# Kernel optimization log

Measured on AMD Instinct MI355X. Metric: run time of the kernel, lower is better.

Reference implementation:

```python
import jax, jax.numpy as jnp
import numpy as np

B, S, D, H = 2, 2048, 1024, 16
HD = D // H

def setup_inputs() -> dict:
    key = jax.random.key(0)
    ks = jax.random.split(key, 9)
    s = 1.0 / np.sqrt(D)
    return {
        "x": jax.random.normal(ks[0], (B, S, D), jnp.float32),
        "Wq": jax.random.normal(ks[1], (D, D), jnp.float32) * s,
        "bq": jnp.zeros((D,), jnp.float32),
        "Wk": jax.random.normal(ks[2], (D, D), jnp.float32) * s,
        "bk": jnp.zeros((D,), jnp.float32),
        "Wv": jax.random.normal(ks[3], (D, D), jnp.float32) * s,
        "bv": jnp.zeros((D,), jnp.float32),
        "Wo": jax.random.normal(ks[4], (D, D), jnp.float32) * s,
        "bo": jnp.zeros((D,), jnp.float32),
    }

def reference(x, Wq, bq, Wk, bk, Wv, bv, Wo, bo):
    b, s, d = x.shape
    def split_heads(t):
        return t.reshape(b, s, H, HD).transpose(0, 2, 1, 3)  # [B,H,S,HD]
    q = split_heads(x @ Wq + bq)
    k = split_heads(x @ Wk + bk)
    v = split_heads(x @ Wv + bv)
    scores = jnp.einsum('bhqd,bhkd->bhqk', q, k) / jnp.sqrt(jnp.float32(HD))
    causal = jnp.tril(jnp.ones((s, s), bool))  # True = keep
    scores = jnp.where(causal, scores, -jnp.inf)
    attn = jax.nn.softmax(scores, axis=-1)
    out = jnp.einsum('bhqk,bhkd->bhqd', attn, v)  # [B,H,S,HD]
    out = out.transpose(0, 2, 1, 3).reshape(b, s, d)
    return out @ Wo + bo
```

## Files before the change

kernel.cpp:

```cpp
#include <hip/hip_runtime.h>

typedef unsigned short u16;
typedef unsigned int u32;
typedef __attribute__((ext_vector_type(8))) short bf16x8;
typedef __attribute__((ext_vector_type(4))) float f32x4;

#define BB 2
#define SS 2048
#define DD 1024
#define HH 16
#define HD 64
#define MM (BB * SS)

__device__ inline float u2f(u32 u) { return __uint_as_float(u); }
__device__ inline u16 f2bf(float f) {
  u32 u = __float_as_uint(f);
  return (u16)((u + 0x7fffu + ((u >> 16) & 1u)) >> 16);
}

__global__ __launch_bounds__(256) void prep(const float* __restrict__ x, u16* __restrict__ xb,
                                            const float* __restrict__ W0, const float* __restrict__ W1,
                                            const float* __restrict__ W2, const float* __restrict__ W3,
                                            u16* __restrict__ Wt) {
  int z = blockIdx.z;
  int t = threadIdx.x;
  if (z >= 4) {
    int gid = (z - 4) * 256 + blockIdx.y * 16 + blockIdx.x;
    int i = (gid * 256 + t) * 8;
    float4 a = *(const float4*)(x + i);
    float4 b = *(const float4*)(x + i + 4);
    uint4 o;
    o.x = (u32)f2bf(a.x) | ((u32)f2bf(a.y) << 16);
    o.y = (u32)f2bf(a.z) | ((u32)f2bf(a.w) << 16);
    o.z = (u32)f2bf(b.x) | ((u32)f2bf(b.y) << 16);
    o.w = (u32)f2bf(b.z) | ((u32)f2bf(b.w) << 16);
    *(uint4*)(xb + i) = o;
    return;
  }
  const float* W = (z == 0) ? W0 : (z == 1) ? W1 : (z == 2) ? W2 : W3;
  u16* out = Wt + (size_t)z * (DD * DD);
  __shared__ __align__(16) u16 T[64][72];
  int n0 = blockIdx.x * 64, k0 = blockIdx.y * 64;
#pragma unroll
  for (int p = 0; p < 4; ++p) {
    int kr = (t >> 4) + p * 16;
    int c4 = (t & 15) * 4;
    float4 v = *(const float4*)&W[(size_t)(k0 + kr) * DD + n0 + c4];
    T[c4 + 0][kr] = f2bf(v.x);
    T[c4 + 1][kr] = f2bf(v.y);
    T[c4 + 2][kr] = f2bf(v.z);
    T[c4 + 3][kr] = f2bf(v.w);
  }
  __syncthreads();
#pragma unroll
  for (int p = 0; p < 2; ++p) {
    int n = (t >> 3) + p * 32;
    int c8 = (t & 7) * 8;
    uint4 v = *(const uint4*)&T[n][c8];
    *(uint4*)&out[(size_t)(n0 + n) * DD + k0 + c8] = v;
  }
}

__global__ __launch_bounds__(256) void gemm_qkv(const u16* __restrict__ xb, const u16* __restrict__ Wt,
                                                const float* __restrict__ bq, const float* __restrict__ bk,
                                                const float* __restrict__ bv,
                                                u16* __restrict__ Qb, u16* __restrict__ Kb, u16* __restrict__ Vtb) {
  __shared__ __align__(16) u16 As[2][128 * 32];
  __shared__ __align__(16) u16 Bs[2][128 * 32];
  const int tid = threadIdx.x, lane = tid & 63, wv = tid >> 6;
  const int wm = (wv >> 1) * 64, wn = (wv & 1) * 64;
  const int l16 = lane & 15, quad = lane >> 4;
  int z = blockIdx.z;
  const u16* Bt = Wt + (size_t)z * (DD * DD);
  const float* bias = (z == 0) ? bq : (z == 1) ? bk : bv;
  int m0 = blockIdx.y * 128, n0 = blockIdx.x * 128;

  const int r0 = tid >> 2, k8 = (tid & 3) << 3;
  const u16* Ap0 = &xb[(size_t)(m0 + r0) * DD + k8];
  const u16* Ap1 = Ap0 + (size_t)64 * DD;
  const u16* Bp0 = &Bt[(size_t)(n0 + r0) * DD + k8];
  const u16* Bp1 = Bp0 + (size_t)64 * DD;

  uint4 a0 = *(const uint4*)Ap0, a1 = *(const uint4*)Ap1;
  uint4 b0 = *(const uint4*)Bp0, b1 = *(const uint4*)Bp1;
  *(uint4*)&As[0][r0 * 32 + k8] = a0;
  *(uint4*)&As[0][(r0 + 64) * 32 + k8] = a1;
  *(uint4*)&Bs[0][r0 * 32 + k8] = b0;
  *(uint4*)&Bs[0][(r0 + 64) * 32 + k8] = b1;
  a0 = *(const uint4*)(Ap0 + 32);
  a1 = *(const uint4*)(Ap1 + 32);
  b0 = *(const uint4*)(Bp0 + 32);
  b1 = *(const uint4*)(Bp1 + 32);
  __syncthreads();

  f32x4 acc[4][4];
  f32x4 zero = {0.f, 0.f, 0.f, 0.f};
#pragma unroll
  for (int i = 0; i < 4; ++i)
#pragma unroll
    for (int j = 0; j < 4; ++j) acc[i][j] = zero;

  for (int kk = 0; kk < 32; ++kk) {
    const int cur = (kk & 1) * 4096;
    bf16x8 af[4], bg[4];
#pragma unroll
    for (int i = 0; i < 4; ++i) {
      af[i] = *(const bf16x8*)&As[0][cur + (wm + i * 16 + l16) * 32 + quad * 8];
      bg[i] = *(const bf16x8*)&Bs[0][cur + (wn + i * 16 + l16) * 32 + quad * 8];
    }
#pragma unroll
    for (int i = 0; i < 4; ++i)
#pragma unroll
      for (int j = 0; j < 4; ++j)
        acc[i][j] = __builtin_amdgcn_mfma_f32_16x16x32_bf16(af[i], bg[j], acc[i][j], 0, 0, 0);
    if (kk + 1 < 32) {
      const int nxt = 4096 - cur;
      *(uint4*)&As[0][nxt + r0 * 32 + k8] = a0;
      *(uint4*)&As[0][nxt + (r0 + 64) * 32 + k8] = a1;
      *(uint4*)&Bs[0][nxt + r0 * 32 + k8] = b0;
      *(uint4*)&Bs[0][nxt + (r0 + 64) * 32 + k8] = b1;
      if (kk + 2 < 32) {
        int ko = (kk + 2) * 32;
        a0 = *(const uint4*)(Ap0 + ko);
        a1 = *(const uint4*)(Ap1 + ko);
        b0 = *(const uint4*)(Bp0 + ko);
        b1 = *(const uint4*)(Bp1 + ko);
      }
    }
    __syncthreads();
  }

  const float qsc = (z == 0) ? 0.180336880f : 1.0f;
  if (z == 2) {
#pragma unroll
    for (int i = 0; i < 4; ++i) {
#pragma unroll
      for (int j = 0; j < 4; ++j) {
        int col = n0 + wn + j * 16 + l16;
        float bcol = bias[col];
        int hh = col >> 6, dd = col & 63;
        int row0 = m0 + wm + i * 16 + quad * 4;
        int bb = row0 >> 11, s0 = row0 & (SS - 1);
        u32 w0 = (u32)f2bf(acc[i][j][0] + bcol) | ((u32)f2bf(acc[i][j][1] + bcol) << 16);
        u32 w1 = (u32)f2bf(acc[i][j][2] + bcol) | ((u32)f2bf(acc[i][j][3] + bcol) << 16);
        uint2 pk; pk.x = w0; pk.y = w1;
        *(uint2*)&Vtb[(((size_t)((bb * HH + hh) * HD + dd)) << 11) + s0] = pk;
      }
    }
  } else {
    u16* out = (z == 0) ? Qb : Kb;
#pragma unroll
    for (int i = 0; i < 4; ++i) {
#pragma unroll
      for (int j = 0; j < 4; ++j) {
        int col = n0 + wn + j * 16 + l16;
        float bcol = bias[col];
        int hh = col >> 6, dd = col & 63;
#pragma unroll
        for (int r = 0; r < 4; ++r) {
          int row = m0 + wm + i * 16 + quad * 4 + r;
          int bb = row >> 11, s = row & (SS - 1);
          out[((size_t)((bb * HH + hh) * SS + s) << 6) | dd] = f2bf((acc[i][j][r] + bcol) * qsc);
        }
      }
    }
  }
}

__global__ __launch_bounds__(256) void gemm_out(const u16* __restrict__ Ub, const u16* __restrict__ Wot,
                                                const float* __restrict__ bo, float* __restrict__ out) {
  __shared__ __align__(16) u16 As[2][128 * 32];
  __shared__ __align__(16) u16 Bs[2][64 * 32];
  const int tid = threadIdx.x, lane = tid & 63, wv = tid >> 6;
  const int wm = (wv >> 1) * 64, wn = (wv & 1) * 32;
  const int l16 = lane & 15, quad = lane >> 4;
  const int r0 = tid >> 2, k8 = (tid & 3) << 3;
  int m0 = blockIdx.y * 128, n0 = blockIdx.x * 64;

  const u16* Ap0 = &Ub[(size_t)(m0 + r0) * DD + k8];
  const u16* Ap1 = Ap0 + (size_t)64 * DD;
  const u16* Bp0 = &Wot[(size_t)(n0 + r0) * DD + k8];

  uint4 a0 = *(const uint4*)Ap0, a1 = *(const uint4*)Ap1, b0 = *(const uint4*)Bp0;
  *(uint4*)&As[0][r0 * 32 + k8] = a0;
  *(uint4*)&As[0][(r0 + 64) * 32 + k8] = a1;
  *(uint4*)&Bs[0][r0 * 32 + k8] = b0;
  a0 = *(const uint4*)(Ap0 + 32);
  a1 = *(const uint4*)(Ap1 + 32);
  b0 = *(const uint4*)(Bp0 + 32);
  __syncthreads();

  f32x4 acc[4][2];
  f32x4 zero = {0.f, 0.f, 0.f, 0.f};
#pragma unroll
  for (int i = 0; i < 4; ++i) { acc[i][0] = zero; acc[i][1] = zero; }

  for (int kk = 0; kk < 32; ++kk) {
    const int curA = (kk & 1) * 4096, curB = (kk & 1) * 2048;
    bf16x8 af[4], bg[2];
#pragma unroll
    for (int i = 0; i < 4; ++i) af[i] = *(const bf16x8*)&As[0][curA + (wm + i * 16 + l16) * 32 + quad * 8];
#pragma unroll
    for (int j = 0; j < 2; ++j) bg[j] = *(const bf16x8*)&Bs[0][curB + (wn + j * 16 + l16) * 32 + quad * 8];
#pragma unroll
    for (int i = 0; i < 4; ++i)
#pragma unroll
      for (int j = 0; j < 2; ++j)
        acc[i][j] = __builtin_amdgcn_mfma_f32_16x16x32_bf16(af[i], bg[j], acc[i][j], 0, 0, 0);
    if (kk + 1 < 32) {
      const int nxtA = 4096 - curA, nxtB = 2048 - curB;
      *(uint4*)&As[0][nxtA + r0 * 32 + k8] = a0;
      *(uint4*)&As[0][nxtA + (r0 + 64) * 32 + k8] = a1;
      *(uint4*)&Bs[0][nxtB + r0 * 32 + k8] = b0;
      if (kk + 2 < 32) {
        int ko = (kk + 2) * 32;
        a0 = *(const uint4*)(Ap0 + ko);
        a1 = *(const uint4*)(Ap1 + ko);
        b0 = *(const uint4*)(Bp0 + ko);
      }
    }
    __syncthreads();
  }

#pragma unroll
  for (int i = 0; i < 4; ++i) {
#pragma unroll
    for (int j = 0; j < 2; ++j) {
      int col = n0 + wn + j * 16 + l16;
      float bcol = bo[col];
#pragma unroll
      for (int r = 0; r < 4; ++r) {
        int row = m0 + wm + i * 16 + quad * 4 + r;
        out[(size_t)row * DD + col] = acc[i][j][r] + bcol;
      }
    }
  }
}

__global__ __launch_bounds__(256, 2) void attention_mfma(const u16* __restrict__ Q, const u16* __restrict__ K,
                                                         const u16* __restrict__ Vt, u16* __restrict__ Uo) {
  const int tid = threadIdx.x, lane = tid & 63, wv = tid >> 6;
  const int l16 = lane & 15, quad = lane >> 4;
  const int h = blockIdx.y, b = blockIdx.z;
  const int qA = blockIdx.x;
  const int qB = 31 - qA;
  const int q0A = qA * 64, q0B = qB * 64;
  const u16* Qh = Q + (size_t)(b * HH + h) * SS * HD;
  const u16* Kh = K + (size_t)(b * HH + h) * SS * HD;
  const u16* Vh = Vt + (size_t)(b * HH + h) * HD * SS;

  __shared__ __align__(16) u16 K_lds[2][64][72];
  __shared__ __align__(16) u16 V_lds[2][64][72];
  __shared__ __align__(16) u16 p_lds[2][64][72];

  bf16x8 qfA0, qfA1, qfB0, qfB1;
  {
    const u16* qa = &Qh[(size_t)(q0A + wv * 16 + l16) * HD + quad * 8];
    qfA0 = *(const bf16x8*)qa;
    qfA1 = *(const bf16x8*)(qa + 32);
    const u16* qb = &Qh[(size_t)(q0B + wv * 16 + l16) * HD + quad * 8];
    qfB0 = *(const bf16x8*)qb;
    qfB1 = *(const bf16x8*)(qb + 32);
  }

  f32x4 zero = {0.f, 0.f, 0.f, 0.f};
  f32x4 oA[4], oB[4];
#pragma unroll
  for (int j = 0; j < 4; ++j) { oA[j] = zero; oB[j] = zero; }
  float lA[4] = {0.f, 0.f, 0.f, 0.f}, lB[4] = {0.f, 0.f, 0.f, 0.f};

  const int sr = tid >> 2, cc = (tid & 3) << 3;
  const u16* Kg = &Kh[(size_t)sr * HD + cc];
  const u16* Vg = &Vh[(size_t)sr * SS + cc];
  const int ktiles = qB + 1;

  uint4 ka = *(const uint4*)Kg, kb = *(const uint4*)(Kg + 32);
  uint4 va = *(const uint4*)Vg, vb = *(const uint4*)(Vg + 32);
  *(uint4*)&K_lds[0][sr][cc] = ka;
  *(uint4*)&K_lds[0][sr][cc + 32] = kb;
  *(uint4*)&V_lds[0][sr][cc] = va;
  *(uint4*)&V_lds[0][sr][cc + 32] = vb;
  {
    const u16* Kn = Kg + (size_t)64 * HD;
    const u16* Vn = Vg + 64;
    ka = *(const uint4*)Kn; kb = *(const uint4*)(Kn + 32);
    va = *(const uint4*)Vn; vb = *(const uint4*)(Vn + 32);
  }
  __syncthreads();

  for (int t = 0; t < ktiles; ++t) {
    const int cur = t & 1;
    const bool doA = (t <= qA);

    f32x4 sA[4], sB[4];
#pragma unroll
    for (int n = 0; n < 4; ++n) {
      bf16x8 kf0 = *(const bf16x8*)&K_lds[cur][n * 16 + l16][quad * 8];
      bf16x8 kf1 = *(const bf16x8*)&K_lds[cur][n * 16 + l16][32 + quad * 8];
      f32x4 aB = zero;
      aB = __builtin_amdgcn_mfma_f32_16x16x32_bf16(qfB0, kf0, aB, 0, 0, 0);
      aB = __builtin_amdgcn_mfma_f32_16x16x32_bf16(qfB1, kf1, aB, 0, 0, 0);
      sB[n] = aB;
      if (doA) {
        f32x4 aA = zero;
        aA = __builtin_amdgcn_mfma_f32_16x16x32_bf16(qfA0, kf0, aA, 0, 0, 0);
        aA = __builtin_amdgcn_mfma_f32_16x16x32_bf16(qfA1, kf1, aA, 0, 0, 0);
        sA[n] = aA;
      }
    }

    {
      const int rel = q0B + wv * 16 + quad * 4 - t * 64;
#pragma unroll
      for (int rr = 0; rr < 4; ++rr) {
        float p0 = __builtin_amdgcn_exp2f(sB[0][rr]);
        float p1 = __builtin_amdgcn_exp2f(sB[1][rr]);
        float p2 = __builtin_amdgcn_exp2f(sB[2][rr]);
        float p3 = __builtin_amdgcn_exp2f(sB[3][rr]);
        if (t == qB) {
          int row = rel + rr;
          p0 = (l16 <= row) ? p0 : 0.f;
          p1 = (16 + l16 <= row) ? p1 : 0.f;
          p2 = (32 + l16 <= row) ? p2 : 0.f;
          p3 = (48 + l16 <= row) ? p3 : 0.f;
        }
        lB[rr] += (p0 + p1) + (p2 + p3);
        u16* pr = p_lds[1][wv * 16 + quad * 4 + rr];
        pr[l16]      = (u16)(__float_as_uint(p0) >> 16);
        pr[16 + l16] = (u16)(__float_as_uint(p1) >> 16);
        pr[32 + l16] = (u16)(__float_as_uint(p2) >> 16);
        pr[48 + l16] = (u16)(__float_as_uint(p3) >> 16);
      }
    }
    if (doA) {
      const int rel = q0A + wv * 16 + quad * 4 - t * 64;
#pragma unroll
      for (int rr = 0; rr < 4; ++rr) {
        float p0 = __builtin_amdgcn_exp2f(sA[0][rr]);
        float p1 = __builtin_amdgcn_exp2f(sA[1][rr]);
        float p2 = __builtin_amdgcn_exp2f(sA[2][rr]);
        float p3 = __builtin_amdgcn_exp2f(sA[3][rr]);
        if (t == qA) {
          int row = rel + rr;
          p0 = (l16 <= row) ? p0 : 0.f;
          p1 = (16 + l16 <= row) ? p1 : 0.f;
          p2 = (32 + l16 <= row) ? p2 : 0.f;
          p3 = (48 + l16 <= row) ? p3 : 0.f;
        }
        lA[rr] += (p0 + p1) + (p2 + p3);
        u16* pr = p_lds[0][wv * 16 + quad * 4 + rr];
        pr[l16]      = (u16)(__float_as_uint(p0) >> 16);
        pr[16 + l16] = (u16)(__float_as_uint(p1) >> 16);
        pr[32 + l16] = (u16)(__float_as_uint(p2) >> 16);
        pr[48 + l16] = (u16)(__float_as_uint(p3) >> 16);
      }
    }

    if (doA) {
      bf16x8 pB0 = *(const bf16x8*)&p_lds[1][wv * 16 + l16][quad * 8];
      bf16x8 pB1 = *(const bf16x8*)&p_lds[1][wv * 16 + l16][32 + quad * 8];
      bf16x8 pA0 = *(const bf16x8*)&p_lds[0][wv * 16 + l16][quad * 8];
      bf16x8 pA1 = *(const bf16x8*)&p_lds[0][wv * 16 + l16][32 + quad * 8];
#pragma unroll
      for (int j = 0; j < 4; ++j) {
        bf16x8 vf0 = *(const bf16x8*)&V_lds[cur][j * 16 + l16][quad * 8];
        bf16x8 vf1 = *(const bf16x8*)&V_lds[cur][j * 16 + l16][32 + quad * 8];
        oB[j] = __builtin_amdgcn_mfma_f32_16x16x32_bf16(pB0, vf0, oB[j], 0, 0, 0);
        oB[j] = __builtin_amdgcn_mfma_f32_16x16x32_bf16(pB1, vf1, oB[j], 0, 0, 0);
        oA[j] = __builtin_amdgcn_mfma_f32_16x16x32_bf16(pA0, vf0, oA[j], 0, 0, 0);
        oA[j] = __builtin_amdgcn_mfma_f32_16x16x32_bf16(pA1, vf1, oA[j], 0, 0, 0);
      }
    } else {
      bf16x8 pB0 = *(const bf16x8*)&p_lds[1][wv * 16 + l16][quad * 8];
      bf16x8 pB1 = *(const bf16x8*)&p_lds[1][wv * 16 + l16][32 + quad * 8];
#pragma unroll
      for (int j = 0; j < 4; ++j) {
        bf16x8 vf0 = *(const bf16x8*)&V_lds[cur][j * 16 + l16][quad * 8];
        bf16x8 vf1 = *(const bf16x8*)&V_lds[cur][j * 16 + l16][32 + quad * 8];
        oB[j] = __builtin_amdgcn_mfma_f32_16x16x32_bf16(pB0, vf0, oB[j], 0, 0, 0);
        oB[j] = __builtin_amdgcn_mfma_f32_16x16x32_bf16(pB1, vf1, oB[j], 0, 0, 0);
      }
    }

    if (t + 1 < ktiles) {
      const int nxt = cur ^ 1;
      *(uint4*)&K_lds[nxt][sr][cc] = ka;
      *(uint4*)&K_lds[nxt][sr][cc + 32] = kb;
      *(uint4*)&V_lds[nxt][sr][cc] = va;
      *(uint4*)&V_lds[nxt][sr][cc + 32] = vb;
      if (t + 2 < ktiles) {
        const u16* Kn = Kg + (size_t)(t + 2) * 64 * HD;
        const u16* Vn = Vg + (t + 2) * 64;
        ka = *(const uint4*)Kn; kb = *(const uint4*)(Kn + 32);
        va = *(const uint4*)Vn; vb = *(const uint4*)(Vn + 32);
      }
    }
    __syncthreads();
  }

#pragma unroll
  for (int rr = 0; rr < 4; ++rr) {
    float a = lA[rr], c = lB[rr];
#pragma unroll
    for (int off = 1; off < 16; off <<= 1) {
      a += __shfl_xor(a, off);
      c += __shfl_xor(c, off);
    }
    lA[rr] = 1.0f / a;
    lB[rr] = 1.0f / c;
  }

#pragma unroll
  for (int j = 0; j < 4; ++j) {
#pragma unroll
    for (int r = 0; r < 4; ++r) {
      int rowA = q0A + wv * 16 + quad * 4 + r;
      int rowB = q0B + wv * 16 + quad * 4 + r;
      Uo[(size_t)(b * SS + rowA) * DD + (h << 6) + j * 16 + l16] = f2bf(oA[j][r] * lA[r]);
      Uo[(size_t)(b * SS + rowB) * DD + (h << 6) + j * 16 + l16] = f2bf(oB[j][r] * lB[r]);
    }
  }
}

extern "C" void kernel_launch(void* const* d_in, const int* in_sizes, int n_in,
                              void* d_out, int out_size, void* d_ws, size_t ws_size,
                              hipStream_t stream) {
  const float* x  = (const float*)d_in[0];
  const float* Wq = (const float*)d_in[1];
  const float* bq = (const float*)d_in[2];
  const float* Wk = (const float*)d_in[3];
  const float* bk = (const float*)d_in[4];
  const float* Wv = (const float*)d_in[5];
  const float* bv = (const float*)d_in[6];
  const float* Wo = (const float*)d_in[7];
  const float* bo = (const float*)d_in[8];
  float* out = (float*)d_out;

  char* ws = (char*)d_ws;
  u16* xb  = (u16*)(ws);
  u16* Wt  = (u16*)(ws + ((size_t)8 << 20));
  u16* Qb  = (u16*)(ws + ((size_t)16 << 20));
  u16* Kb  = (u16*)(ws + ((size_t)24 << 20));
  u16* Vtb = (u16*)(ws + ((size_t)32 << 20));
  u16* Ub  = (u16*)(ws + ((size_t)40 << 20));

  prep<<<dim3(16, 16, 12), dim3(256), 0, stream>>>(x, xb, Wq, Wk, Wv, Wo, Wt);
  gemm_qkv<<<dim3(8, 32, 3), dim3(256), 0, stream>>>(xb, Wt, bq, bk, bv, Qb, Kb, Vtb);
  attention_mfma<<<dim3(16, 16, 2), dim3(256), 0, stream>>>(Qb, Kb, Vtb, Ub);
  gemm_out<<<dim3(16, 32), dim3(256), 0, stream>>>(Ub, Wt + (size_t)3 * DD * DD, bo, out);
}
```

Baseline: 189.8 us.

## Remap blocks for XCD-aware L2 locality, swizzle attention K/V LDS, raise occupancy

Flattens the grids of both GEMMs and the attention kernel and decodes block ids so that tiles sharing the same A or B panels, or the same batch-head, land on the same XCD. The aim is better L2 reuse across the MI355X's chiplets. The attention K/V shared tiles drop the padded 72-wide rows for an XOR-swizzled 64-wide layout, which cuts LDS footprint and avoids bank conflicts. Launch bounds are raised to 3 blocks per CU, which may force register spills.

```diff
diff --git a/kernel.cpp b/kernel.cpp
--- a/kernel.cpp
+++ b/kernel.cpp
@@ -17,6 +17,8 @@
   u32 u = __float_as_uint(f);
   return (u16)((u + 0x7fffu + ((u >> 16) & 1u)) >> 16);
 }
+
+__device__ inline int sw(int r, int ci) { return r * 64 + (((ci ^ (r & 7)) & 7) << 3); }
 
 __global__ __launch_bounds__(256) void prep(const float* __restrict__ x, u16* __restrict__ xb,
                                             const float* __restrict__ W0, const float* __restrict__ W1,
@@ -61,19 +63,25 @@
   }
 }
 
-__global__ __launch_bounds__(256) void gemm_qkv(const u16* __restrict__ xb, const u16* __restrict__ Wt,
-                                                const float* __restrict__ bq, const float* __restrict__ bk,
-                                                const float* __restrict__ bv,
-                                                u16* __restrict__ Qb, u16* __restrict__ Kb, u16* __restrict__ Vtb) {
+__global__ __launch_bounds__(256, 3) void gemm_qkv(const u16* __restrict__ xb, const u16* __restrict__ Wt,
+                                                   const float* __restrict__ bq, const float* __restrict__ bk,
+                                                   const float* __restrict__ bv,
+                                                   u16* __restrict__ Qb, u16* __restrict__ Kb, u16* __restrict__ Vtb) {
   __shared__ __align__(16) u16 As[2][128 * 32];
   __shared__ __align__(16) u16 Bs[2][128 * 32];
   const int tid = threadIdx.x, lane = tid & 63, wv = tid >> 6;
   const int wm = (wv >> 1) * 64, wn = (wv & 1) * 64;
   const int l16 = lane & 15, quad = lane >> 4;
-  int z = blockIdx.z;
+
+  const int id = blockIdx.x;
+  const int xcd = id & 7, inner = id >> 3;
+  const int mg = xcd >> 1, ng = xcd & 1;
+  const int im = inner & 7, rest = inner >> 3;
+  const int in_ = rest & 3, z = rest >> 2;
+  const int m0 = (mg * 8 + im) * 128, n0 = (ng * 4 + in_) * 128;
+
   const u16* Bt = Wt + (size_t)z * (DD * DD);
   const float* bias = (z == 0) ? bq : (z == 1) ? bk : bv;
-  int m0 = blockIdx.y * 128, n0 = blockIdx.x * 128;
 
   const int r0 = tid >> 2, k8 = (tid & 3) << 3;
   const u16* Ap0 = &xb[(size_t)(m0 + r0) * DD + k8];
@@ -167,15 +175,20 @@
   }
 }
 
-__global__ __launch_bounds__(256) void gemm_out(const u16* __restrict__ Ub, const u16* __restrict__ Wot,
-                                                const float* __restrict__ bo, float* __restrict__ out) {
+__global__ __launch_bounds__(256, 3) void gemm_out(const u16* __restrict__ Ub, const u16* __restrict__ Wot,
+                                                   const float* __restrict__ bo, float* __restrict__ out) {
   __shared__ __align__(16) u16 As[2][128 * 32];
   __shared__ __align__(16) u16 Bs[2][64 * 32];
   const int tid = threadIdx.x, lane = tid & 63, wv = tid >> 6;
   const int wm = (wv >> 1) * 64, wn = (wv & 1) * 32;
   const int l16 = lane & 15, quad = lane >> 4;
   const int r0 = tid >> 2, k8 = (tid & 3) << 3;
-  int m0 = blockIdx.y * 128, n0 = blockIdx.x * 64;
+
+  const int id = blockIdx.x;
+  const int xcd = id & 7, inner = id >> 3;
+  const int mg = xcd >> 1, ng = xcd & 1;
+  const int im = inner & 7, in_ = inner >> 3;
+  const int m0 = (mg * 8 + im) * 128, n0 = (ng * 8 + in_) * 64;
 
   const u16* Ap0 = &Ub[(size_t)(m0 + r0) * DD + k8];
   const u16* Ap1 = Ap0 + (size_t)64 * DD;
@@ -237,20 +250,21 @@
   }
 }
 
-__global__ __launch_bounds__(256, 2) void attention_mfma(const u16* __restrict__ Q, const u16* __restrict__ K,
+__global__ __launch_bounds__(256, 3) void attention_mfma(const u16* __restrict__ Q, const u16* __restrict__ K,
                                                          const u16* __restrict__ Vt, u16* __restrict__ Uo) {
   const int tid = threadIdx.x, lane = tid & 63, wv = tid >> 6;
   const int l16 = lane & 15, quad = lane >> 4;
-  const int h = blockIdx.y, b = blockIdx.z;
-  const int qA = blockIdx.x;
+  const int bh = blockIdx.x & 31;
+  const int b = bh >> 4, h = bh & 15;
+  const int qA = blockIdx.x >> 5;
   const int qB = 31 - qA;
   const int q0A = qA * 64, q0B = qB * 64;
   const u16* Qh = Q + (size_t)(b * HH + h) * SS * HD;
   const u16* Kh = K + (size_t)(b * HH + h) * SS * HD;
   const u16* Vh = Vt + (size_t)(b * HH + h) * HD * SS;
 
-  __shared__ __align__(16) u16 K_lds[2][64][72];
-  __shared__ __align__(16) u16 V_lds[2][64][72];
+  __shared__ __align__(16) u16 K_lds[2][64 * 64];
+  __shared__ __align__(16) u16 V_lds[2][64 * 64];
   __shared__ __align__(16) u16 p_lds[2][64][72];
 
   bf16x8 qfA0, qfA1, qfB0, qfB1;
@@ -269,17 +283,19 @@
   for (int j = 0; j < 4; ++j) { oA[j] = zero; oB[j] = zero; }
   float lA[4] = {0.f, 0.f, 0.f, 0.f}, lB[4] = {0.f, 0.f, 0.f, 0.f};
 
-  const int sr = tid >> 2, cc = (tid & 3) << 3;
+  const int sr = tid >> 2, ci = tid & 3;
+  const int cc = ci << 3;
   const u16* Kg = &Kh[(size_t)sr * HD + cc];
   const u16* Vg = &Vh[(size_t)sr * SS + cc];
   const int ktiles = qB + 1;
+  const int wlo = sw(sr, ci), whi = sw(sr, ci + 4);
 
   uint4 ka = *(const uint4*)Kg, kb = *(const uint4*)(Kg + 32);
   uint4 va = *(const uint4*)Vg, vb = *(const uint4*)(Vg + 32);
-  *(uint4*)&K_lds[0][sr][cc] = ka;
-  *(uint4*)&K_lds[0][sr][cc + 32] = kb;
-  *(uint4*)&V_lds[0][sr][cc] = va;
-  *(uint4*)&V_lds[0][sr][cc + 32] = vb;
+  *(uint4*)&K_lds[0][wlo] = ka;
+  *(uint4*)&K_lds[0][whi] = kb;
+  *(uint4*)&V_lds[0][wlo] = va;
+  *(uint4*)&V_lds[0][whi] = vb;
   {
     const u16* Kn = Kg + (size_t)64 * HD;
     const u16* Vn = Vg + 64;
@@ -295,8 +311,9 @@
     f32x4 sA[4], sB[4];
 #pragma unroll
     for (int n = 0; n < 4; ++n) {
-      bf16x8 kf0 = *(const bf16x8*)&K_lds[cur][n * 16 + l16][quad * 8];
-      bf16x8 kf1 = *(const bf16x8*)&K_lds[cur][n * 16 + l16][32 + quad * 8];
+      const int kr = n * 16 + l16;
+      bf16x8 kf0 = *(const bf16x8*)&K_lds[cur][sw(kr, quad)];
+      bf16x8 kf1 = *(const bf16x8*)&K_lds[cur][sw(kr, quad + 4)];
       f32x4 aB = zero;
       aB = __builtin_amdgcn_mfma_f32_16x16x32_bf16(qfB0, kf0, aB, 0, 0, 0);
       aB = __builtin_amdgcn_mfma_f32_16x16x32_bf16(qfB1, kf1, aB, 0, 0, 0);
@@ -363,8 +380,9 @@
       bf16x8 pA1 = *(const bf16x8*)&p_lds[0][wv * 16 + l16][32 + quad * 8];
 #pragma unroll
       for (int j = 0; j < 4; ++j) {
-        bf16x8 vf0 = *(const bf16x8*)&V_lds[cur][j * 16 + l16][quad * 8];
-        bf16x8 vf1 = *(const bf16x8*)&V_lds[cur][j * 16 + l16][32 + quad * 8];
+        const int vr = j * 16 + l16;
+        bf16x8 vf0 = *(const bf16x8*)&V_lds[cur][sw(vr, quad)];
+        bf16x8 vf1 = *(const bf16x8*)&V_lds[cur][sw(vr, quad + 4)];
         oB[j] = __builtin_amdgcn_mfma_f32_16x16x32_bf16(pB0, vf0, oB[j], 0, 0, 0);
         oB[j] = __builtin_amdgcn_mfma_f32_16x16x32_bf16(pB1, vf1, oB[j], 0, 0, 0);
         oA[j] = __builtin_amdgcn_mfma_f32_16x16x32_bf16(pA0, vf0, oA[j], 0, 0, 0);
@@ -375,8 +393,9 @@
       bf16x8 pB1 = *(const bf16x8*)&p_lds[1][wv * 16 + l16][32 + quad * 8];
 #pragma unroll
       for (int j = 0; j < 4; ++j) {
-        bf16x8 vf0 = *(const bf16x8*)&V_lds[cur][j * 16 + l16][quad * 8];
-        bf16x8 vf1 = *(const bf16x8*)&V_lds[cur][j * 16 + l16][32 + quad * 8];
+        const int vr = j * 16 + l16;
+        bf16x8 vf0 = *(const bf16x8*)&V_lds[cur][sw(vr, quad)];
+        bf16x8 vf1 = *(const bf16x8*)&V_lds[cur][sw(vr, quad + 4)];
         oB[j] = __builtin_amdgcn_mfma_f32_16x16x32_bf16(pB0, vf0, oB[j], 0, 0, 0);
         oB[j] = __builtin_amdgcn_mfma_f32_16x16x32_bf16(pB1, vf1, oB[j], 0, 0, 0);
       }
@@ -384,10 +403,10 @@
 
     if (t + 1 < ktiles) {
       const int nxt = cur ^ 1;
-      *(uint4*)&K_lds[nxt][sr][cc] = ka;
-      *(uint4*)&K_lds[nxt][sr][cc + 32] = kb;
-      *(uint4*)&V_lds[nxt][sr][cc] = va;
-      *(uint4*)&V_lds[nxt][sr][cc + 32] = vb;
+      *(uint4*)&K_lds[nxt][wlo] = ka;
+      *(uint4*)&K_lds[nxt][whi] = kb;
+      *(uint4*)&V_lds[nxt][wlo] = va;
+      *(uint4*)&V_lds[nxt][whi] = vb;
       if (t + 2 < ktiles) {
         const u16* Kn = Kg + (size_t)(t + 2) * 64 * HD;
         const u16* Vn = Vg + (t + 2) * 64;
@@ -445,7 +464,7 @@
   u16* Ub  = (u16*)(ws + ((size_t)40 << 20));
 
   prep<<<dim3(16, 16, 12), dim3(256), 0, stream>>>(x, xb, Wq, Wk, Wv, Wo, Wt);
-  gemm_qkv<<<dim3(8, 32, 3), dim3(256), 0, stream>>>(xb, Wt, bq, bk, bv, Qb, Kb, Vtb);
-  attention_mfma<<<dim3(16, 16, 2), dim3(256), 0, stream>>>(Qb, Kb, Vtb, Ub);
-  gemm_out<<<dim3(16, 32), dim3(256), 0, stream>>>(Ub, Wt + (size_t)3 * DD * DD, bo, out);
-}
+  gemm_qkv<<<dim3(768), dim3(256), 0, stream>>>(xb, Wt, bq, bk, bv, Qb, Kb, Vtb);
+  attention_mfma<<<dim3(512), dim3(256), 0, stream>>>(Qb, Kb, Vtb, Ub);
+  gemm_out<<<dim3(512), dim3(256), 0, stream>>>(Ub, Wt + (size_t)3 * DD * DD, bo, out);
+}
```

Result: slower. 195.9 us (+3.2%).
